# Kernel tuning notes

Measured on AMD Instinct MI355X. Metric: run time of the kernel, lower is better.

Reference implementation:

```python
import jax, jax.numpy as jnp
import numpy as np

DIM = 1024
N_HEADS = 16
HD = DIM // N_HEADS


def setup_inputs() -> dict:
    key = jax.random.key(0)
    k1, k2, k3 = jax.random.split(key, 3)
    x = jax.random.normal(k1, (4, 2048, DIM), dtype=jnp.float32)
    # torch nn.Linear weights: W_qkv [3*dim, dim], W_proj [dim, dim]; y = x @ W.T
    W_qkv = jax.random.normal(k2, (3 * DIM, DIM), dtype=jnp.float32) * 0.02
    W_proj = jax.random.normal(k3, (DIM, DIM), dtype=jnp.float32) * 0.02
    return {"x": x, "W_qkv": W_qkv, "W_proj": W_proj}


def reference(x, W_qkv, W_proj):
    B, T, D = x.shape
    H, hd = N_HEADS, HD
    # fused QKV projection: (B,T,3D)
    qkv = jnp.einsum('btd,ed->bte', x, W_qkv)
    # view(B,T,3,H,hd).transpose(1,2) -> (B,3,T,H,hd)
    qkv = qkv.reshape(B, T, 3, H, hd).transpose(0, 2, 1, 3, 4)
    q, k, v = qkv[:, 0], qkv[:, 1], qkv[:, 2]  # each (B,T,H,hd)
    # NOTE: faithful to source — SDPA sees (B,T) as batch dims and attends
    # over the heads axis (length H), NOT the sequence axis.
    scale = 1.0 / np.sqrt(hd).astype(np.float32)
    scores = jnp.einsum('btie,btje->btij', q, k) * scale  # (B,T,H,H)
    attn = jax.nn.softmax(scores, axis=-1)
    out = jnp.einsum('btij,btje->btie', attn, v)  # (B,T,H,hd)
    # out.transpose(1,2).contiguous().view(B,T,D)
    out = out.transpose(0, 2, 1, 3).reshape(B, T, D)
    return jnp.einsum('btd,ed->bte', out, W_proj)
```

## Files before the change

kernel.cpp:

```cpp
#include <hip/hip_runtime.h>


typedef __bf16 bf16x8 __attribute__((ext_vector_type(8)));
typedef float  f32x16 __attribute__((ext_vector_type(16)));

typedef __attribute__((address_space(3))) void       lds_void;
typedef const __attribute__((address_space(1))) void gbl_void;

__device__ __forceinline__ unsigned short f2b(float f) {
    unsigned int u = __builtin_bit_cast(unsigned int, f);
    return (unsigned short)((u + 0x7FFFu + ((u >> 16) & 1u)) >> 16);
}
__device__ __forceinline__ unsigned int pack2(float a, float b) {
    return (unsigned int)f2b(a) | ((unsigned int)f2b(b) << 16);
}
__device__ __forceinline__ void unpack8(uint4 u, float* f) {
    unsigned int w[4] = {u.x, u.y, u.z, u.w};
#pragma unroll
    for (int a = 0; a < 4; ++a) {
        union { unsigned int i; float f; } lo, hi;
        lo.i = w[a] << 16;
        hi.i = w[a] & 0xFFFF0000u;
        f[a * 2]     = lo.f;
        f[a * 2 + 1] = hi.f;
    }
}

__global__ __launch_bounds__(256) void cvt_all(const float* __restrict__ x,
                                               const float* __restrict__ wqkv,
                                               const float* __restrict__ wproj,
                                               unsigned short* __restrict__ xb,
                                               unsigned short* __restrict__ wqkvb,
                                               unsigned short* __restrict__ wprojb) {
    int i = blockIdx.x * 256 + threadIdx.x;
    const float* src;
    unsigned short* dst;
    if (i < 2097152)      { src = x;     dst = xb;                   }
    else if (i < 2883584) { src = wqkv;  dst = wqkvb;  i -= 2097152; }
    else                  { src = wproj; dst = wprojb; i -= 2883584; }
    float4 f = reinterpret_cast<const float4*>(src)[i];
    ushort4 u;
    u.x = f2b(f.x); u.y = f2b(f.y); u.z = f2b(f.z); u.w = f2b(f.w);
    reinterpret_cast<ushort4*>(dst)[i] = u;
}

__device__ __forceinline__ void store_c(float* C, long idx, float v)          { C[idx] = v; }
__device__ __forceinline__ void store_c(unsigned short* C, long idx, float v) { C[idx] = f2b(v); }

template <int BM, typename CT>
__global__ __launch_bounds__(256) void gemm_bt(const unsigned short* __restrict__ A,
                                               const unsigned short* __restrict__ B,
                                               CT* __restrict__ C,
                                               int M, int N, int K) {
    constexpr int MI = BM / 64;
    __shared__ __align__(16) unsigned short As[BM * 64];
    __shared__ __align__(16) unsigned short Bs[128 * 64];

    const int tid  = threadIdx.x;
    const int lane = tid & 63;
    const int wave = tid >> 6;
    const long bm  = blockIdx.y;
    const long bn  = blockIdx.x;
    const int wm   = (wave >> 1) * (BM / 2);
    const int wn   = (wave & 1) * 64;

    f32x16 acc[MI][2] = {};

    const unsigned short* Ab = A + bm * BM * (long)K;
    const unsigned short* Bb = B + bn * 128 * (long)K;

    const int srow  = tid >> 3;
    const int sgcol = ((tid & 7) ^ (srow & 7)) << 3;

    for (int k0 = 0; k0 < K; k0 += 64) {
#pragma unroll
        for (int r = 0; r < BM / 32; ++r)
            __builtin_amdgcn_global_load_lds(
                (gbl_void*)(Ab + (long)(r * 32 + srow) * K + k0 + sgcol),
                (lds_void*)(As + (r * 256 + wave * 64) * 8), 16, 0, 0);
#pragma unroll
        for (int r = 0; r < 4; ++r)
            __builtin_amdgcn_global_load_lds(
                (gbl_void*)(Bb + (long)(r * 32 + srow) * K + k0 + sgcol),
                (lds_void*)(Bs + (r * 256 + wave * 64) * 8), 16, 0, 0);
        __syncthreads();

        const int arow = lane & 31;
        const int kh   = lane >> 5;
#pragma unroll
        for (int kk = 0; kk < 4; ++kk) {
            const int c  = kk * 2 + kh;
            const int sw = (c ^ (lane & 7)) << 3;
            bf16x8 af[MI], bfr[2];
#pragma unroll
            for (int i = 0; i < MI; ++i)
                af[i] = *reinterpret_cast<const bf16x8*>(As + (wm + i * 32 + arow) * 64 + sw);
#pragma unroll
            for (int j = 0; j < 2; ++j)
                bfr[j] = *reinterpret_cast<const bf16x8*>(Bs + (wn + j * 32 + arow) * 64 + sw);
#pragma unroll
            for (int i = 0; i < MI; ++i)
#pragma unroll
                for (int j = 0; j < 2; ++j)
                    acc[i][j] = __builtin_amdgcn_mfma_f32_32x32x16_bf16(af[i], bfr[j], acc[i][j], 0, 0, 0);
        }
        __syncthreads();
    }

    const long mbase = bm * BM + wm + ((lane >> 5) << 2);
    const long nbase = bn * 128 + wn + (lane & 31);
#pragma unroll
    for (int i = 0; i < MI; ++i)
#pragma unroll
        for (int j = 0; j < 2; ++j)
#pragma unroll
            for (int r = 0; r < 16; ++r) {
                const long row = mbase + i * 32 + (r & 3) + 8 * (r >> 2);
                store_c(C, row * (long)N + nbase + j * 32, acc[i][j][r]);
            }
}

__global__ __launch_bounds__(256) void attn_rowlocal(const unsigned short* __restrict__ qkv,
                                                     unsigned short* __restrict__ out3) {
    __shared__ __align__(16) unsigned short rows[4 * 3072];
    __shared__ float attnS[4][16][17];

    const int tid  = threadIdx.x;
    const int lane = tid & 63;
    const int wave = tid >> 6;
    const int m0   = blockIdx.x * 4;

    {
        const uint4* src = reinterpret_cast<const uint4*>(qkv + (long)m0 * 3072);
        uint4* dst = reinterpret_cast<uint4*>(rows);
#pragma unroll
        for (int c = 0; c < 6; ++c) {
            const int S  = c * 256 + tid;
            const int gs = (S & ~7) | ((S & 7) ^ ((S >> 3) & 7));
            dst[S] = src[gs];
        }
    }
    __syncthreads();

    const int m = m0 + wave;
    const int b = m >> 11;
    const int t = m & 2047;
    const unsigned short* rw = rows + wave * 3072;

    const int i  = lane & 15;
    const int j0 = (lane >> 4) << 2;
    float sc[4] = {0.f, 0.f, 0.f, 0.f};
#pragma unroll
    for (int c8 = 0; c8 < 8; ++c8) {
        uint4 qu = *reinterpret_cast<const uint4*>(rw + i * 64 + ((c8 ^ (i & 7)) << 3));
        float qf[8];
        unpack8(qu, qf);
#pragma unroll
        for (int jj = 0; jj < 4; ++jj) {
            const int vi = 16 + j0 + jj;
            uint4 ku = *reinterpret_cast<const uint4*>(rw + vi * 64 + ((c8 ^ (vi & 7)) << 3));
            float kf[8];
            unpack8(ku, kf);
#pragma unroll
            for (int d = 0; d < 8; ++d) sc[jj] += qf[d] * kf[d];
        }
    }
#pragma unroll
    for (int jj = 0; jj < 4; ++jj) sc[jj] *= 0.125f;

    float mx = fmaxf(fmaxf(sc[0], sc[1]), fmaxf(sc[2], sc[3]));
    mx = fmaxf(mx, __shfl_xor(mx, 16));
    mx = fmaxf(mx, __shfl_xor(mx, 32));
    float sum = 0.f;
#pragma unroll
    for (int jj = 0; jj < 4; ++jj) { sc[jj] = __expf(sc[jj] - mx); sum += sc[jj]; }
    sum += __shfl_xor(sum, 16);
    sum += __shfl_xor(sum, 32);
    const float inv = 1.0f / sum;
#pragma unroll
    for (int jj = 0; jj < 4; ++jj) attnS[wave][i][j0 + jj] = sc[jj] * inv;
    __syncthreads();

    const int oi = lane >> 2;
    const int s0 = (lane & 3) << 4;
    const int c0 = (lane & 3) << 1;
    float o[16];
#pragma unroll
    for (int ss = 0; ss < 16; ++ss) o[ss] = 0.f;
#pragma unroll
    for (int j = 0; j < 16; ++j) {
        const float a  = attnS[wave][oi][j];
        const int   vi = 32 + j;
        uint4 v0 = *reinterpret_cast<const uint4*>(rw + vi * 64 + (((c0)     ^ (vi & 7)) << 3));
        uint4 v1 = *reinterpret_cast<const uint4*>(rw + vi * 64 + (((c0 + 1) ^ (vi & 7)) << 3));
        float vf[16];
        unpack8(v0, vf);
        unpack8(v1, vf + 8);
#pragma unroll
        for (int ss = 0; ss < 16; ++ss) o[ss] += a * vf[ss];
    }

    uint4 r0, r1;
    r0.x = pack2(o[0],  o[1]);  r0.y = pack2(o[2],  o[3]);
    r0.z = pack2(o[4],  o[5]);  r0.w = pack2(o[6],  o[7]);
    r1.x = pack2(o[8],  o[9]);  r1.y = pack2(o[10], o[11]);
    r1.z = pack2(o[12], o[13]); r1.w = pack2(o[14], o[15]);

    const long base = (long)b * (2048 * 1024)
                    + (long)(oi * 128 + (t >> 4)) * 1024
                    + 64 * (t & 15) + s0;
    *reinterpret_cast<uint4*>(out3 + base)     = r0;
    *reinterpret_cast<uint4*>(out3 + base + 8) = r1;
}

extern "C" void kernel_launch(void* const* d_in, const int* in_sizes, int n_in,
                              void* d_out, int out_size, void* d_ws, size_t ws_size,
                              hipStream_t stream) {
    const float* x     = (const float*)d_in[0];
    const float* Wqkv  = (const float*)d_in[1];
    const float* Wproj = (const float*)d_in[2];
    float* out = (float*)d_out;

    char* ws = (char*)d_ws;
    unsigned short* xb     = (unsigned short*)(ws);
    unsigned short* wqkvb  = (unsigned short*)(ws + 16777216);
    unsigned short* wprojb = (unsigned short*)(ws + 23068672);
    unsigned short* qkvb   = (unsigned short*)(ws + 25165824);
    unsigned short* out3b  = (unsigned short*)(ws + 75497472);

    cvt_all<<<dim3(12288), dim3(256), 0, stream>>>(x, Wqkv, Wproj, xb, wqkvb, wprojb);

    gemm_bt<128, unsigned short><<<dim3(24, 64), dim3(256), 0, stream>>>(
        xb, wqkvb, qkvb, 8192, 3072, 1024);

    attn_rowlocal<<<dim3(2048), dim3(256), 0, stream>>>(qkvb, out3b);

    gemm_bt<64, float><<<dim3(8, 128), dim3(256), 0, stream>>>(
        out3b, wprojb, out, 8192, 1024, 1024);
}
```

Baseline: 193.8 us.

## Use 256x256 double-buffered direct-to-LDS GEMM kernel for QKV projection

Adds a new 512-thread GEMM kernel with 256x256 output tiles, double-buffered LDS staging via global_load_lds with XOR swizzle, and a barrier-interleaved schedule of LDS reads, MFMA bursts and async prefetch. It replaces the 128-row tile kernel for the large QKV projection. The aim is more data reuse per block and better overlap of loads with MFMA work. The cost is only 384 blocks, which may leave the GPU underfilled, plus many barriers and a large LDS footprint.

```diff
diff --git a/kernel.cpp b/kernel.cpp
--- a/kernel.cpp
+++ b/kernel.cpp
@@ -47,6 +47,141 @@
 __device__ __forceinline__ void store_c(float* C, long idx, float v)          { C[idx] = v; }
 __device__ __forceinline__ void store_c(unsigned short* C, long idx, float v) { C[idx] = f2b(v); }
 
+__device__ __forceinline__ void stage_tile(const unsigned short* __restrict__ Gbase,
+                                           unsigned short* Lbase,
+                                           long K, int kt, int tid) {
+    const int wave = tid >> 6;
+    const int c    = ((tid & 7) ^ ((tid >> 3) & 7)) << 3;
+    const unsigned short* g = Gbase + (long)(tid >> 3) * K + (long)kt * 64 + c;
+    unsigned short* l = Lbase + wave * 512;
+#pragma unroll
+    for (int j = 0; j < 4; ++j)
+        __builtin_amdgcn_global_load_lds((gbl_void*)(g + (long)j * 64 * K),
+                                         (lds_void*)(l + j * 4096), 16, 0, 0);
+}
+
+template <typename CT>
+__global__ __launch_bounds__(512, 2) void gemm256(const unsigned short* __restrict__ A,
+                                                  const unsigned short* __restrict__ B,
+                                                  CT* __restrict__ C,
+                                                  int M, int N, int K) {
+    __shared__ __align__(16) unsigned short sA[2][16384];
+    __shared__ __align__(16) unsigned short sB[2][16384];
+
+    const int tid  = threadIdx.x;
+    const int lane = tid & 63;
+    const int wave = tid >> 6;
+    const int wm   = wave >> 2;
+    const int wn   = wave & 3;
+    const long bm  = blockIdx.y;
+    const long bn  = blockIdx.x;
+
+    const unsigned short* Ab = A + bm * 256 * (long)K;
+    const unsigned short* Bb = B + bn * 256 * (long)K;
+
+    f32x16 acc[4][2] = {};
+    const int NT = K >> 6;
+
+    stage_tile(Bb, &sB[0][0], K, 0, tid);
+    stage_tile(Ab, &sA[0][0], K, 0, tid);
+    stage_tile(Bb, &sB[1][0], K, 1, tid);
+    stage_tile(Ab, &sA[1][0], K, 1, tid);
+    asm volatile("s_waitcnt vmcnt(8)" ::: "memory");
+    __builtin_amdgcn_s_barrier();
+
+    const int arow = lane & 31;
+    const int kh   = lane >> 5;
+    const int sx   = lane & 7;
+
+    bf16x8 af[2][4], b0[4], b1[4];
+
+    auto read_a = [&](int q, int half) {
+#pragma unroll
+        for (int f = 0; f < 2; ++f)
+#pragma unroll
+            for (int kk = 0; kk < 4; ++kk)
+                af[f][kk] = *reinterpret_cast<const bf16x8*>(
+                    &sA[q][(wm * 128 + half * 64 + f * 32 + arow) * 64 +
+                           (((kk * 2 + kh) ^ sx) << 3)]);
+    };
+    auto read_b = [&](int q, int half, bf16x8 (&bs)[4]) {
+#pragma unroll
+        for (int kk = 0; kk < 4; ++kk)
+            bs[kk] = *reinterpret_cast<const bf16x8*>(
+                &sB[q][(wn * 64 + half * 32 + arow) * 64 +
+                       (((kk * 2 + kh) ^ sx) << 3)]);
+    };
+    auto mfma2 = [&](f32x16& c0, f32x16& c1, bf16x8 (&bs)[4]) {
+        __builtin_amdgcn_s_setprio(1);
+#pragma unroll
+        for (int kk = 0; kk < 4; ++kk) {
+            c0 = __builtin_amdgcn_mfma_f32_32x32x16_bf16(af[0][kk], bs[kk], c0, 0, 0, 0);
+            c1 = __builtin_amdgcn_mfma_f32_32x32x16_bf16(af[1][kk], bs[kk], c1, 0, 0, 0);
+        }
+        __builtin_amdgcn_s_setprio(0);
+    };
+
+    for (int it = 0; it < NT / 2; ++it) {
+        const int t0 = it * 2;
+        read_a(0, 0);
+        read_b(0, 0, b0);
+        __builtin_amdgcn_s_barrier();
+        mfma2(acc[0][0], acc[1][0], b0);
+        __builtin_amdgcn_s_barrier();
+        read_b(0, 1, b1);
+        __builtin_amdgcn_s_barrier();
+        mfma2(acc[0][1], acc[1][1], b1);
+        __builtin_amdgcn_s_barrier();
+        read_a(0, 1);
+        if (t0 + 2 < NT) stage_tile(Bb, &sB[0][0], K, t0 + 2, tid);
+        __builtin_amdgcn_s_barrier();
+        mfma2(acc[2][1], acc[3][1], b1);
+        __builtin_amdgcn_s_barrier();
+        if (t0 + 2 < NT) {
+            stage_tile(Ab, &sA[0][0], K, t0 + 2, tid);
+            asm volatile("s_waitcnt vmcnt(8)" ::: "memory");
+        } else {
+            asm volatile("s_waitcnt vmcnt(0)" ::: "memory");
+        }
+        __builtin_amdgcn_s_barrier();
+        mfma2(acc[2][0], acc[3][0], b0);
+        __builtin_amdgcn_s_barrier();
+        read_a(1, 0);
+        read_b(1, 0, b0);
+        __builtin_amdgcn_s_barrier();
+        mfma2(acc[0][0], acc[1][0], b0);
+        __builtin_amdgcn_s_barrier();
+        read_b(1, 1, b1);
+        __builtin_amdgcn_s_barrier();
+        mfma2(acc[0][1], acc[1][1], b1);
+        __builtin_amdgcn_s_barrier();
+        read_a(1, 1);
+        if (t0 + 3 < NT) stage_tile(Bb, &sB[1][0], K, t0 + 3, tid);
+        __builtin_amdgcn_s_barrier();
+        mfma2(acc[2][1], acc[3][1], b1);
+        __builtin_amdgcn_s_barrier();
+        if (t0 + 3 < NT) {
+            stage_tile(Ab, &sA[1][0], K, t0 + 3, tid);
+            asm volatile("s_waitcnt vmcnt(8)" ::: "memory");
+        }
+        __builtin_amdgcn_s_barrier();
+        mfma2(acc[2][0], acc[3][0], b0);
+        __builtin_amdgcn_s_barrier();
+    }
+
+    const long mb = bm * 256 + wm * 128 + ((lane >> 5) << 2);
+    const long nb = bn * 256 + wn * 64 + (lane & 31);
+#pragma unroll
+    for (int f = 0; f < 4; ++f)
+#pragma unroll
+        for (int n = 0; n < 2; ++n)
+#pragma unroll
+            for (int r = 0; r < 16; ++r) {
+                const long row = mb + f * 32 + (r & 3) + 8 * (r >> 2);
+                store_c(C, row * (long)N + nb + n * 32, acc[f][n][r]);
+            }
+}
+
 template <int BM, typename CT>
 __global__ __launch_bounds__(256) void gemm_bt(const unsigned short* __restrict__ A,
                                                const unsigned short* __restrict__ B,
@@ -230,7 +365,7 @@
 
     cvt_all<<<dim3(12288), dim3(256), 0, stream>>>(x, Wqkv, Wproj, xb, wqkvb, wprojb);
 
-    gemm_bt<128, unsigned short><<<dim3(24, 64), dim3(256), 0, stream>>>(
+    gemm256<unsigned short><<<dim3(12, 32), dim3(512), 0, stream>>>(
         xb, wqkvb, qkvb, 8192, 3072, 1024);
 
     attn_rowlocal<<<dim3(2048), dim3(256), 0, stream>>>(qkvb, out3b);
```

Result: slower. 214.5 us (+10.7%).

## Replace GEMM with double-buffered 256x128 pipelined kernel using 16x16 MFMA

Applied to the files above, without the earlier changes.

Swaps the simple single-buffered GEMM for one with 512-thread blocks, 256x128 tiles, double-buffered LDS stages prefetched two k-steps ahead, and register double-buffering of A fragments, so that global loads, LDS reads and MFMA overlap. It uses 16x16x32 MFMA with s_setprio around the compute, explicit waitcnt/barrier scheduling, and an XCD-aware block swizzle for L2 locality. Both the QKV and output projections use it. The cost is more LDS and registers per block, and the hand-written wait counts are fragile.

```diff
diff --git a/kernel.cpp b/kernel.cpp
--- a/kernel.cpp
+++ b/kernel.cpp
@@ -2,7 +2,7 @@
 
 
 typedef __bf16 bf16x8 __attribute__((ext_vector_type(8)));
-typedef float  f32x16 __attribute__((ext_vector_type(16)));
+typedef float  f32x4  __attribute__((ext_vector_type(4)));
 
 typedef __attribute__((address_space(3))) void       lds_void;
 typedef const __attribute__((address_space(1))) void gbl_void;
@@ -47,77 +47,133 @@
 __device__ __forceinline__ void store_c(float* C, long idx, float v)          { C[idx] = v; }
 __device__ __forceinline__ void store_c(unsigned short* C, long idx, float v) { C[idx] = f2b(v); }
 
-template <int BM, typename CT>
-__global__ __launch_bounds__(256) void gemm_bt(const unsigned short* __restrict__ A,
-                                               const unsigned short* __restrict__ B,
-                                               CT* __restrict__ C,
-                                               int M, int N, int K) {
-    constexpr int MI = BM / 64;
-    __shared__ __align__(16) unsigned short As[BM * 64];
-    __shared__ __align__(16) unsigned short Bs[128 * 64];
+#define BAR    __builtin_amdgcn_s_barrier()
+#define LGK0   asm volatile("s_waitcnt lgkmcnt(0)" ::: "memory")
+#define VMC(n) asm volatile("s_waitcnt vmcnt(" #n ")" ::: "memory")
+
+template <typename CT>
+__global__ __launch_bounds__(512, 2) void gemm_pl(const unsigned short* __restrict__ A,
+                                                  const unsigned short* __restrict__ B,
+                                                  CT* __restrict__ C,
+                                                  int M, int N, int K, int NBX) {
+    __shared__ __align__(16) unsigned short sA[2][16384];
+    __shared__ __align__(16) unsigned short sB[2][8192];
 
     const int tid  = threadIdx.x;
     const int lane = tid & 63;
     const int wave = tid >> 6;
-    const long bm  = blockIdx.y;
-    const long bn  = blockIdx.x;
-    const int wm   = (wave >> 1) * (BM / 2);
+    const int wm   = (wave >> 1) * 64;
     const int wn   = (wave & 1) * 64;
 
-    f32x16 acc[MI][2] = {};
-
-    const unsigned short* Ab = A + bm * BM * (long)K;
+    const int nwg = gridDim.x;
+    const int cpx = nwg >> 3;
+    const int swz = ((int)blockIdx.x & 7) * cpx + ((int)blockIdx.x >> 3);
+    const long bm = swz / NBX;
+    const long bn = swz % NBX;
+
+    const unsigned short* Ab = A + bm * 256 * (long)K;
     const unsigned short* Bb = B + bn * 128 * (long)K;
 
-    const int srow  = tid >> 3;
-    const int sgcol = ((tid & 7) ^ (srow & 7)) << 3;
-
-    for (int k0 = 0; k0 < K; k0 += 64) {
-#pragma unroll
-        for (int r = 0; r < BM / 32; ++r)
-            __builtin_amdgcn_global_load_lds(
-                (gbl_void*)(Ab + (long)(r * 32 + srow) * K + k0 + sgcol),
-                (lds_void*)(As + (r * 256 + wave * 64) * 8), 16, 0, 0);
-#pragma unroll
-        for (int r = 0; r < 4; ++r)
-            __builtin_amdgcn_global_load_lds(
-                (gbl_void*)(Bb + (long)(r * 32 + srow) * K + k0 + sgcol),
-                (lds_void*)(Bs + (r * 256 + wave * 64) * 8), 16, 0, 0);
-        __syncthreads();
-
-        const int arow = lane & 31;
-        const int kh   = lane >> 5;
-#pragma unroll
-        for (int kk = 0; kk < 4; ++kk) {
-            const int c  = kk * 2 + kh;
-            const int sw = (c ^ (lane & 7)) << 3;
-            bf16x8 af[MI], bfr[2];
-#pragma unroll
-            for (int i = 0; i < MI; ++i)
-                af[i] = *reinterpret_cast<const bf16x8*>(As + (wm + i * 32 + arow) * 64 + sw);
-#pragma unroll
-            for (int j = 0; j < 2; ++j)
-                bfr[j] = *reinterpret_cast<const bf16x8*>(Bs + (wn + j * 32 + arow) * 64 + sw);
-#pragma unroll
-            for (int i = 0; i < MI; ++i)
-#pragma unroll
-                for (int j = 0; j < 2; ++j)
-                    acc[i][j] = __builtin_amdgcn_mfma_f32_32x32x16_bf16(af[i], bfr[j], acc[i][j], 0, 0, 0);
-        }
-        __syncthreads();
-    }
-
-    const long mbase = bm * BM + wm + ((lane >> 5) << 2);
-    const long nbase = bn * 128 + wn + (lane & 31);
-#pragma unroll
-    for (int i = 0; i < MI; ++i)
+    const int NT = K >> 6;
+
+    f32x4 acc[4][4] = {};
+
+    const int sr = tid >> 3;
+    const int sc = ((tid & 7) ^ (sr & 7)) << 3;
+
+    auto stageA = [&](int p, int t) {
+        const unsigned short* g = Ab + (long)sr * K + (long)t * 64 + sc;
+        unsigned short* l = &sA[p][0] + wave * 512;
+#pragma unroll
+        for (int j = 0; j < 4; ++j)
+            __builtin_amdgcn_global_load_lds((gbl_void*)(g + (long)j * 64 * K),
+                                             (lds_void*)(l + j * 4096), 16, 0, 0);
+    };
+    auto stageB = [&](int p, int t) {
+        const unsigned short* g = Bb + (long)sr * K + (long)t * 64 + sc;
+        unsigned short* l = &sB[p][0] + wave * 512;
 #pragma unroll
         for (int j = 0; j < 2; ++j)
-#pragma unroll
-            for (int r = 0; r < 16; ++r) {
-                const long row = mbase + i * 32 + (r & 3) + 8 * (r >> 2);
-                store_c(C, row * (long)N + nbase + j * 32, acc[i][j][r]);
-            }
+            __builtin_amdgcn_global_load_lds((gbl_void*)(g + (long)j * 64 * K),
+                                             (lds_void*)(l + j * 4096), 16, 0, 0);
+    };
+
+    const int fr = lane & 15;
+    const int fk = lane >> 4;
+
+    bf16x8 af[4][2], afn[4][2], b01[2][2], b23[2][2];
+
+    auto rdA = [&](bf16x8 (&dst)[4][2], int p) {
+#pragma unroll
+        for (int mt = 0; mt < 4; ++mt) {
+            const int row = wm + mt * 16 + fr;
+#pragma unroll
+            for (int h = 0; h < 2; ++h)
+                dst[mt][h] = *reinterpret_cast<const bf16x8*>(
+                    &sA[p][row * 64 + (((h * 4 + fk) ^ (row & 7)) << 3)]);
+        }
+    };
+    auto rdB = [&](bf16x8 (&dst)[2][2], int p, int nbase) {
+#pragma unroll
+        for (int nt = 0; nt < 2; ++nt) {
+            const int row = wn + (nbase + nt) * 16 + fr;
+#pragma unroll
+            for (int h = 0; h < 2; ++h)
+                dst[nt][h] = *reinterpret_cast<const bf16x8*>(
+                    &sB[p][row * 64 + (((h * 4 + fk) ^ (row & 7)) << 3)]);
+        }
+    };
+    auto mm16 = [&](bf16x8 (&a)[4][2], bf16x8 (&b)[2][2], int nbase) {
+        __builtin_amdgcn_s_setprio(1);
+#pragma unroll
+        for (int mt = 0; mt < 4; ++mt)
+#pragma unroll
+            for (int nt = 0; nt < 2; ++nt)
+#pragma unroll
+                for (int h = 0; h < 2; ++h)
+                    acc[mt][nbase + nt] = __builtin_amdgcn_mfma_f32_16x16x32_bf16(
+                        a[mt][h], b[nt][h], acc[mt][nbase + nt], 0, 0, 0);
+        __builtin_amdgcn_s_setprio(0);
+    };
+
+    stageA(0, 0); stageB(0, 0);
+    stageA(1, 1); stageB(1, 1);
+    VMC(6);
+    BAR;
+    rdA(af, 0); rdB(b01, 0, 0);
+    LGK0;
+    BAR;
+
+    for (int u = 0; u < NT; ++u) {
+        const int p = u & 1;
+        const int t2 = (u + 2 < NT) ? (u + 2) : (NT - 1);
+        stageA(p, t2);
+        rdB(b23, p, 2);
+        mm16(af, b01, 0);
+        LGK0;
+        VMC(4);
+        BAR;
+        stageB(p, t2);
+        if (u + 1 < NT) { rdA(afn, p ^ 1); rdB(b01, p ^ 1, 0); }
+        mm16(af, b23, 2);
+        LGK0;
+        BAR;
+#pragma unroll
+        for (int mt = 0; mt < 4; ++mt)
+#pragma unroll
+            for (int h = 0; h < 2; ++h)
+                af[mt][h] = afn[mt][h];
+    }
+
+    const long mb = bm * 256 + wm + (fk << 2);
+    const long nb = bn * 128 + wn + fr;
+#pragma unroll
+    for (int mt = 0; mt < 4; ++mt)
+#pragma unroll
+        for (int nt = 0; nt < 4; ++nt)
+#pragma unroll
+            for (int r = 0; r < 4; ++r)
+                store_c(C, (mb + mt * 16 + r) * (long)N + nb + nt * 16, acc[mt][nt][r]);
 }
 
 __global__ __launch_bounds__(256) void attn_rowlocal(const unsigned short* __restrict__ qkv,
@@ -230,11 +286,11 @@
 
     cvt_all<<<dim3(12288), dim3(256), 0, stream>>>(x, Wqkv, Wproj, xb, wqkvb, wprojb);
 
-    gemm_bt<128, unsigned short><<<dim3(24, 64), dim3(256), 0, stream>>>(
-        xb, wqkvb, qkvb, 8192, 3072, 1024);
+    gemm_pl<unsigned short><<<dim3(768), dim3(512), 0, stream>>>(
+        xb, wqkvb, qkvb, 8192, 3072, 1024, 24);
 
     attn_rowlocal<<<dim3(2048), dim3(256), 0, stream>>>(qkvb, out3b);
 
-    gemm_bt<64, float><<<dim3(8, 128), dim3(256), 0, stream>>>(
-        out3b, wprojb, out, 8192, 1024, 1024);
-}
+    gemm_pl<float><<<dim3(256), dim3(512), 0, stream>>>(
+        out3b, wprojb, out, 8192, 1024, 1024, 8);
+}
```

New measurement: 231.0 us. 19.2% more time.
